# Optimization experiments

Hardware: AMD Instinct MI355X
Metric: run time of the kernel (lower is better)

Reference implementation:

```python
import jax, jax.numpy as jnp
import numpy as np
from jax import lax

C = 256
HEADS = 8
HD = C // HEADS  # 32
D = 32  # max(L=32, C//16)
KERNELS = [1, 3, 5, 7]
EPS = 1e-5


def setup_inputs() -> dict:
    key = jax.random.key(0)
    ks = jax.random.split(key, 16)
    inp = {
        'x': jax.random.normal(ks[0], (8, C, 32, 32), jnp.float32),
        'qkv_w': jax.random.normal(ks[1], (3 * C, C), jnp.float32) * 0.05,
        'out_w': jax.random.normal(ks[2], (C, C), jnp.float32) * 0.05,
        'conv_w1': jax.random.normal(ks[3], (C, C, 1, 1), jnp.float32) * 0.05,
        'conv_w3': jax.random.normal(ks[4], (C, C, 3, 3), jnp.float32) * 0.05,
        'conv_w5': jax.random.normal(ks[5], (C, C, 5, 5), jnp.float32) * 0.05,
        'conv_w7': jax.random.normal(ks[6], (C, C, 7, 7), jnp.float32) * 0.05,
        'conv_b': jax.random.normal(ks[7], (4, C), jnp.float32) * 0.05,
        'bn_gamma': jax.random.uniform(ks[8], (4, C), jnp.float32, 0.5, 1.5),
        'bn_beta': jax.random.normal(ks[9], (4, C), jnp.float32) * 0.05,
        'bn_mean': jax.random.normal(ks[10], (4, C), jnp.float32) * 0.05,
        'bn_var': jax.random.uniform(ks[11], (4, C), jnp.float32, 0.5, 1.5),
        'fc_w': jax.random.normal(ks[12], (D, C), jnp.float32) * 0.05,
        'fc_b': jax.random.normal(ks[13], (D,), jnp.float32) * 0.05,
        'fcs_w': jax.random.normal(ks[14], (4, C, D), jnp.float32) * 0.05,
        'fcs_b': jax.random.normal(ks[15], (4, C), jnp.float32) * 0.05,
    }
    return inp


def _conv_bn_relu(x, w, b, g, beta, m, v):
    k = w.shape[-1]
    y = lax.conv_general_dilated(
        x, w, window_strides=(1, 1), padding=[(k // 2, k // 2)] * 2,
        dimension_numbers=('NCHW', 'OIHW', 'NCHW'))
    y = y + b[None, :, None, None]
    inv = g / jnp.sqrt(v + EPS)  # eval-mode batchnorm
    y = y * inv[None, :, None, None] + (beta - m * inv)[None, :, None, None]
    return jax.nn.relu(y)


def reference(x, qkv_w, out_w, conv_w1, conv_w3, conv_w5, conv_w7, conv_b,
              bn_gamma, bn_beta, bn_mean, bn_var, fc_w, fc_b, fcs_w, fcs_b):
    bsz, ch, ht, wd = x.shape
    n = ht * wd
    xf = x.reshape(bsz, ch, n)
    qkv = jnp.einsum('oc,bcn->bon', qkv_w, xf)  # [b, 3C, N] (1x1 conv)
    q, k, v = jnp.split(qkv, 3, axis=1)
    q = q.reshape(bsz, HEADS, HD, n)
    k = k.reshape(bsz, HEADS, HD, n)
    v = v.reshape(bsz, HEADS, HD, n)
    scale = 1.0 / np.sqrt(HD)
    scores = jnp.einsum('bhdi,bhdj->bhij', q, k) * scale  # [b,h,N,N]
    probs = jax.nn.softmax(scores, axis=-1)
    ctx = jnp.einsum('bhij,bhdj->bhdi', probs, v)  # [b,h,hd,N]
    ctx = ctx.reshape(bsz, ch, ht, wd)
    out = jnp.einsum('oc,bcn->bon', out_w, ctx.reshape(bsz, ch, n)).reshape(bsz, ch, ht, wd)

    ws = [conv_w1, conv_w3, conv_w5, conv_w7]
    feats = jnp.stack([
        _conv_bn_relu(out, ws[i], conv_b[i], bn_gamma[i], bn_beta[i], bn_mean[i], bn_var[i])
        for i in range(4)
    ], axis=0)  # [4, b, C, H, W]
    U = feats.sum(axis=0)
    S = U.mean(axis=(-2, -1))  # [b, C]
    Z = S @ fc_w.T + fc_b  # [b, D]
    logits = jnp.einsum('kcd,bd->kbc', fcs_w, Z) + fcs_b[:, None, :]  # [4,b,C]
    attn = jax.nn.softmax(logits, axis=0)[:, :, :, None, None]  # softmax over kernel branches
    V = (attn * feats).sum(axis=0)  # [b, C, H, W]
    return V
```

## Files before the change

kernel.cpp:

```cpp
#include <hip/hip_runtime.h>
#include <math.h>


typedef __attribute__((ext_vector_type(8))) short bf16x8;
typedef __attribute__((ext_vector_type(4))) float f32x4;

__device__ __forceinline__ ushort f2bf(float f) {
  uint32_t u = __float_as_uint(f);
  u += 0x7fffu + ((u >> 16) & 1u);
  return (ushort)(u >> 16);
}

__device__ __forceinline__ uint cvt_pk(float lo, float hi) {
  uint r;
  asm volatile("v_cvt_pk_bf16_f32 %0, %1, %2" : "=v"(r) : "v"(lo), "v"(hi));
  return r;
}


template <int KK>
__device__ __forceinline__ void repack_dev(const float* __restrict__ src,
                                           ushort* __restrict__ dst, int M, int co,
                                           char* smraw) {
  ushort(*t)[KK + 1] = (ushort(*)[KK + 1])smraw;
  int tid = threadIdx.x;
  for (int idx = tid; idx < 256 * KK; idx += 256) {
    int ci = idx / KK, k = idx - ci * KK;
    t[ci][k] = f2bf(src[(size_t)co * 256 * KK + idx]);
  }
  __syncthreads();
  for (int idx = tid; idx < 256 * KK; idx += 256) {
    int k = idx >> 8, ci = idx & 255;
    dst[((size_t)k * M + co) * 256 + ci] = t[ci][k];
  }
}

__device__ __forceinline__ void pad_dev(const float* __restrict__ src,
                                        ushort* __restrict__ dst, int y, int b,
                                        char* smraw) {
  ushort(*t)[258] = (ushort(*)[258])smraw;
  int tid = threadIdx.x;
  for (int u = 0; u < 32; ++u) {
    int idx = u * 256 + tid;
    int c = idx >> 5, p = idx & 31;
    t[p][c] = f2bf(src[(((size_t)b * 256 + c) << 10) + (y << 5) + p]);
  }
  __syncthreads();
  for (int u = 0; u < 32; ++u) {
    int idx = u * 256 + tid;
    int p = idx >> 8, c = idx & 255;
    dst[(((size_t)b * 38 + y + 3) * 38 + p + 3) * 256 + c] = t[p][c];
  }
}

__global__ __launch_bounds__(256) void prep_all(
    const float* __restrict__ qkv_w, const float* __restrict__ out_w,
    const float* __restrict__ cw1, const float* __restrict__ cw3,
    const float* __restrict__ cw5, const float* __restrict__ cw7,
    ushort* __restrict__ Wq, ushort* __restrict__ Wo, ushort* __restrict__ Wc,
    const float* __restrict__ x, ushort* __restrict__ P1,
    const float* __restrict__ cb, const float* __restrict__ g,
    const float* __restrict__ be, const float* __restrict__ mn,
    const float* __restrict__ v, float* __restrict__ binv, float* __restrict__ bb2) {
  __shared__ __align__(16) char sm[25600];
  int gx = blockIdx.x;
  if (gx < 768) repack_dev<1>(qkv_w, Wq, 768, gx, sm);
  else if (gx < 1024) repack_dev<1>(out_w, Wo, 256, gx - 768, sm);
  else if (gx < 1280) repack_dev<1>(cw1, Wc, 256, gx - 1024, sm);
  else if (gx < 1536) repack_dev<9>(cw3, Wc + 65536, 256, gx - 1280, sm);
  else if (gx < 1792) repack_dev<25>(cw5, Wc + 655360, 256, gx - 1536, sm);
  else if (gx < 2048) repack_dev<49>(cw7, Wc + 2293760, 256, gx - 1792, sm);
  else if (gx < 2304) pad_dev(x, P1, (gx - 2048) & 31, (gx - 2048) >> 5, sm);
  else {
    int tid = threadIdx.x;
#pragma unroll
    for (int u = 0; u < 4; ++u) {
      int i = u * 256 + tid;
      float inv = g[i] * rsqrtf(v[i] + 1e-5f);
      binv[i] = inv;
      bb2[i] = be[i] + (cb[i] - mn[i]) * inv;
    }
  }
}

template <int MODE>
__device__ __forceinline__ void conv_core(
    const ushort* __restrict__ W, const ushort* __restrict__ X,
    float* __restrict__ outF, ushort* __restrict__ outU,
    int M, int KS, int b, int co0, int pxt, int cs0, int cs1, bool accum,
    char* smem) {
  const int R = KS >> 1;
  const int NT = KS * KS;
  const int NR = 4 + 2 * R;
  const int NPIX = NR * 38;
  char* Bs = smem;
  char* As = smem + 24320;
  const int tid = threadIdx.x;
  const int w = tid >> 6, l = tid & 63, lr = l & 15, sg = l >> 4;
  const int y0 = pxt * 4;
  const ushort* Xb = X + ((size_t)b * 38 + (y0 + 3 - R)) * 38 * 256;

  f32x4 acc[4][4] = {};

  auto stageA = [&](int t, int ci0, int bufsel) {
    const ushort* Wt = W + ((size_t)t * M + co0) * 256 + ci0;
    char* dbase = As + (bufsel << 13) + (w << 11);
#pragma unroll
    for (int u = 0; u < 2; ++u) {
      int idx16 = (w * 2 + u) * 64 + l;
      int co = idx16 >> 2, s = idx16 & 3;
      const ushort* src = Wt + (size_t)co * 256 + ((s ^ ((co >> 1) & 3)) << 3);
      __builtin_amdgcn_global_load_lds(
          (const __attribute__((address_space(1))) void*)src,
          (__attribute__((address_space(3))) void*)(dbase + (u << 10)), 16, 0, 0);
    }
  };

  int g = 0;
  stageA(0, cs0 << 5, 0);
  const int u_stg = (NPIX * 4 + 255) >> 8;
  for (int cs = cs0; cs < cs1; ++cs) {
    int ci0 = cs << 5;
    for (int u = 0; u < u_stg; ++u) {
      int idx = (u << 8) + tid;
      if (idx < NPIX * 4) {
        int pix = idx >> 2, s = idx & 3;
        int pr = pix / 38, pc = pix - pr * 38;
        const ushort* srcp = Xb + ((size_t)(pr * 38 + pc)) * 256 + ci0 +
                             ((s ^ ((pc >> 1) & 3)) << 3);
        __builtin_amdgcn_global_load_lds(
            (const __attribute__((address_space(1))) void*)srcp,
            (__attribute__((address_space(3))) void*)(Bs + (u << 12) + (w << 10)),
            16, 0, 0);
      }
    }
    __syncthreads();
    int dy = 0, dx = 0;
    for (int t = 0; t < NT; ++t) {
      bool staged = true;
      if (t + 1 < NT) stageA(t + 1, ci0, (g + 1) & 1);
      else if (cs + 1 < cs1) stageA(0, ci0 + 32, (g + 1) & 1);
      else staged = false;
      if (staged)
        asm volatile("s_waitcnt vmcnt(2)\n\ts_barrier" ::: "memory");
      else
        asm volatile("s_waitcnt vmcnt(0)\n\ts_barrier" ::: "memory");

      bf16x8 af[4], bfr[4];
      char* Ab = As + ((g & 1) << 13);
#pragma unroll
      for (int fa = 0; fa < 4; ++fa) {
        int co = (w & 1) * 64 + fa * 16 + lr;
        af[fa] = *(const bf16x8*)(Ab + (co << 6) + ((sg ^ ((co >> 1) & 3)) << 4));
      }
      int rowbase = (w >> 1) * 2 + dy;
      int cbase = dx + 3 - R + lr;
#pragma unroll
      for (int fp = 0; fp < 4; ++fp) {
        int lrow = rowbase + (fp >> 1);
        int pc = cbase + ((fp & 1) << 4);
        bfr[fp] = *(const bf16x8*)(Bs + ((lrow * 38 + pc) << 6) +
                                   ((sg ^ ((pc >> 1) & 3)) << 4));
      }
      __builtin_amdgcn_s_setprio(1);
#pragma unroll
      for (int fa = 0; fa < 4; ++fa)
#pragma unroll
        for (int fp = 0; fp < 4; ++fp)
          acc[fa][fp] = __builtin_amdgcn_mfma_f32_16x16x32_bf16(
              af[fa], bfr[fp], acc[fa][fp], 0, 0, 0);
      __builtin_amdgcn_s_setprio(0);
      ++g;
      if (++dx == KS) { dx = 0; ++dy; }
      asm volatile("s_barrier" ::: "memory");
    }
  }
  int coB = co0 + (w & 1) * 64;
  int pxB = pxt * 128 + (w >> 1) * 64;
#pragma unroll
  for (int fa = 0; fa < 4; ++fa) {
#pragma unroll
    for (int fp = 0; fp < 4; ++fp) {
      int px = pxB + (fp >> 1) * 32 + (fp & 1) * 16 + lr;
      int cobase = coB + fa * 16 + 4 * sg;
      f32x4 v4 = acc[fa][fp];
      if (MODE == 2) {
#pragma unroll
        for (int r = 0; r < 4; ++r) {
          int co = cobase + r;
          float* dst = &outF[((size_t)b * M + co) * 1024 + px];
          if (accum) unsafeAtomicAdd(dst, v4[r]);
          else *dst = v4[r];
        }
      } else if (MODE == 1) {
        int y = px >> 5, x = px & 31;
        ushort* dst = outU + ((size_t)(b * 38 + y + 3) * 38 + x + 3) * 256 + cobase;
        *(uint*)dst = cvt_pk(v4[0], v4[1]);
        *(uint*)(dst + 2) = cvt_pk(v4[2], v4[3]);
      } else {
        if (coB < 256) {
          int h = cobase >> 5, d = cobase & 31;
          ushort* dst = outU + ((size_t)(b * 8 + h) * 1024 + px) * 32 + d;
          const float sc = 0.17677669529663687f;
          *(uint*)dst = cvt_pk(v4[0] * sc, v4[1] * sc);
          *(uint*)(dst + 2) = cvt_pk(v4[2] * sc, v4[3] * sc);
        } else if (coB < 512) {
          int c2 = cobase - 256;
          int h = c2 >> 5, d = c2 & 31;
          ushort* dst = outU + 2097152 + ((size_t)(b * 8 + h) * 1024 + px) * 32 + d;
          *(uint*)dst = cvt_pk(v4[0], v4[1]);
          *(uint*)(dst + 2) = cvt_pk(v4[2], v4[3]);
        } else {
          int c2 = cobase - 512;
#pragma unroll
          for (int r = 0; r < 4; ++r)
            outU[4194304 + ((size_t)(b * 256 + c2 + r)) * 1024 + px] = f2bf(v4[r]);
        }
      }
    }
  }
}

__global__ __launch_bounds__(256, 2) void gemm_qkv(const ushort* __restrict__ W,
                                                   const ushort* __restrict__ X,
                                                   ushort* __restrict__ U) {
  __shared__ __align__(16) char smem[40704];
  int cot = blockIdx.x >> 3, pxt = blockIdx.x & 7, b = blockIdx.y;
  conv_core<0>(W, X, nullptr, U, 768, 1, b, cot * 128, pxt, 0, 8, false, smem);
}

__global__ __launch_bounds__(256, 2) void gemm_oproj(const ushort* __restrict__ W,
                                                     const ushort* __restrict__ X,
                                                     ushort* __restrict__ U) {
  __shared__ __align__(16) char smem[40704];
  int cot = blockIdx.x >> 3, pxt = blockIdx.x & 7, b = blockIdx.y;
  conv_core<1>(W, X, nullptr, U, 256, 1, b, cot * 128, pxt, 0, 8, false, smem);
}

__global__ __launch_bounds__(256, 4) void conv_fused(const ushort* __restrict__ Wc,
                                                     const ushort* __restrict__ X,
                                                     float* __restrict__ feats) {
  __shared__ __align__(16) char smem[40704];
  int gx = blockIdx.x;
  int sub = gx & 127;
  int pxt = sub & 7, cot = (sub >> 3) & 1, b = sub >> 4;
  int br, cs0, cs1;
  if (gx < 512) {
    br = 3; int ch = gx >> 7; cs0 = ch * 2; cs1 = cs0 + 2;
  } else if (gx < 768) {
    br = 2; int ch = (gx >> 7) & 1; cs0 = ch * 4; cs1 = cs0 + 4;
  } else {
    br = 1; int ch = (gx >> 7) & 1; cs0 = ch * 4; cs1 = cs0 + 4;
  }
  const int ksarr[4] = {1, 3, 5, 7};
  const int wofs[4] = {0, 65536, 655360, 2293760};
  conv_core<2>(Wc + wofs[br], X, feats + (size_t)br * 2097152, nullptr, 256,
               ksarr[br], b, cot * 128, pxt, cs0, cs1, true, smem);
  if (gx >= 768 && gx < 896) {
    __syncthreads();
    conv_core<2>(Wc, X, feats, nullptr, 256, 1, b, cot * 128, pxt, 0, 8, false,
                 smem);
  }
}

__global__ __launch_bounds__(256, 2) void flash_attn(const ushort* __restrict__ QKV,
                                                     ushort* __restrict__ P2out) {
  __shared__ __align__(16) char smem[24576];
  const int tid = threadIdx.x, w = tid >> 6, l = tid & 63, lr = l & 15, sg = l >> 4;
  char* Ks = smem;
  char* Vs = smem + 4096;
  char* Ps = smem + 8192 + (w << 12);
  int bh = blockIdx.y, b = bh >> 3, h = bh & 7;
  const ushort* QT = QKV + (size_t)bh * 32768;
  const ushort* KT = QKV + 2097152 + (size_t)bh * 32768;
  const ushort* VT = QKV + 4194304 + (size_t)(b * 256 + h * 32) * 1024;
  int ibase = blockIdx.x * 128 + w * 32;

  bf16x8 qf[2];
#pragma unroll
  for (int i16 = 0; i16 < 2; ++i16)
    qf[i16] = *(const bf16x8*)(QT + ((size_t)(ibase + i16 * 16 + lr)) * 32 + sg * 8);

  f32x4 oacc[4] = {};
  float mrow[2] = {-3e30f, -3e30f};
  float lrow[2] = {0.f, 0.f};

  for (int jb = 0; jb < 1024; jb += 64) {
    {
      int j = tid >> 2, s = tid & 3;
      const ushort* srcK = KT + (size_t)(jb + j) * 32 + ((s ^ ((j >> 1) & 3)) << 3);
      __builtin_amdgcn_global_load_lds(
          (const __attribute__((address_space(1))) void*)srcK,
          (__attribute__((address_space(3))) void*)(Ks + (w << 10)), 16, 0, 0);
      int d = tid >> 3, s2 = tid & 7;
      const ushort* srcV = VT + (size_t)d * 1024 + jb + ((s2 ^ (d & 7)) << 3);
      __builtin_amdgcn_global_load_lds(
          (const __attribute__((address_space(1))) void*)srcV,
          (__attribute__((address_space(3))) void*)(Vs + (w << 10)), 16, 0, 0);
    }
    __syncthreads();

    bf16x8 kf[4];
#pragma unroll
    for (int jt = 0; jt < 4; ++jt) {
      int j = jt * 16 + lr;
      kf[jt] = *(const bf16x8*)(Ks + j * 64 + ((sg ^ ((j >> 1) & 3)) << 4));
    }
    f32x4 sac[2][4] = {};
#pragma unroll
    for (int i16 = 0; i16 < 2; ++i16)
#pragma unroll
      for (int jt = 0; jt < 4; ++jt)
        sac[i16][jt] = __builtin_amdgcn_mfma_f32_16x16x32_bf16(
            kf[jt], qf[i16], sac[i16][jt], 0, 0, 0);

#pragma unroll
    for (int i16 = 0; i16 < 2; ++i16) {
      float tmax = sac[i16][0][0];
#pragma unroll
      for (int jt = 0; jt < 4; ++jt)
#pragma unroll
        for (int r = 0; r < 4; ++r) tmax = fmaxf(tmax, sac[i16][jt][r]);
      tmax = fmaxf(tmax, __shfl_xor(tmax, 16));
      tmax = fmaxf(tmax, __shfl_xor(tmax, 32));
      float mnew = fmaxf(mrow[i16], tmax);
      float fac = __expf(mrow[i16] - mnew);
      mrow[i16] = mnew;
      float psum = 0.f;
      int i = i16 * 16 + lr;
      char* prow = Ps + i * 128;
#pragma unroll
      for (int jt = 0; jt < 4; ++jt) {
        float p0 = __expf(sac[i16][jt][0] - mnew);
        float p1 = __expf(sac[i16][jt][1] - mnew);
        float p2 = __expf(sac[i16][jt][2] - mnew);
        float p3 = __expf(sac[i16][jt][3] - mnew);
        psum += (p0 + p1) + (p2 + p3);
        int j0 = jt * 16 + sg * 4;
        uint* dst = (uint*)(prow + (((j0 >> 3) ^ (i & 7)) << 4) + ((j0 & 7) << 1));
        dst[0] = cvt_pk(p0, p1);
        dst[1] = cvt_pk(p2, p3);
      }
      lrow[i16] = lrow[i16] * fac + psum;
#pragma unroll
      for (int d16 = 0; d16 < 2; ++d16)
#pragma unroll
        for (int r = 0; r < 4; ++r) oacc[d16 * 2 + i16][r] *= fac;
    }
    asm volatile("s_waitcnt lgkmcnt(0)" ::: "memory");

#pragma unroll
    for (int h2 = 0; h2 < 2; ++h2) {
      bf16x8 vf[2], pf[2];
#pragma unroll
      for (int d16 = 0; d16 < 2; ++d16) {
        int d = d16 * 16 + lr;
        vf[d16] = *(const bf16x8*)(Vs + d * 128 + ((((h2 << 2) + sg) ^ (d & 7)) << 4));
      }
#pragma unroll
      for (int i16 = 0; i16 < 2; ++i16) {
        int i = i16 * 16 + lr;
        pf[i16] = *(const bf16x8*)(Ps + i * 128 + ((((h2 << 2) + sg) ^ (i & 7)) << 4));
      }
#pragma unroll
      for (int d16 = 0; d16 < 2; ++d16)
#pragma unroll
        for (int i16 = 0; i16 < 2; ++i16)
          oacc[d16 * 2 + i16] = __builtin_amdgcn_mfma_f32_16x16x32_bf16(
              vf[d16], pf[i16], oacc[d16 * 2 + i16], 0, 0, 0);
    }
    __syncthreads();
  }

  float linv[2];
#pragma unroll
  for (int i16 = 0; i16 < 2; ++i16) {
    float lt = lrow[i16];
    lt += __shfl_xor(lt, 16);
    lt += __shfl_xor(lt, 32);
    linv[i16] = 1.0f / lt;
  }
#pragma unroll
  for (int i16 = 0; i16 < 2; ++i16) {
    int i = ibase + i16 * 16 + lr;
    int y = i >> 5, x = i & 31;
    ushort* dst0 = P2out + ((size_t)(b * 38 + y + 3) * 38 + x + 3) * 256 + h * 32 + sg * 4;
#pragma unroll
    for (int d16 = 0; d16 < 2; ++d16) {
      f32x4 v = oacc[d16 * 2 + i16];
      ushort* dst = dst0 + d16 * 16;
      *(uint*)dst = cvt_pk(v[0] * linv[i16], v[1] * linv[i16]);
      *(uint*)(dst + 2) = cvt_pk(v[2] * linv[i16], v[3] * linv[i16]);
    }
  }
}

__global__ __launch_bounds__(256) void reduce_s(const float* __restrict__ feats,
                                                const float* __restrict__ binv,
                                                const float* __restrict__ bb2,
                                                float* __restrict__ S) {
  int bc = blockIdx.x;
  int c = bc & 255;
  const float* p = feats + (size_t)bc * 1024;
  float s = 0;
#pragma unroll
  for (int k = 0; k < 4; ++k) {
    float bi = binv[k * 256 + c], bo = bb2[k * 256 + c];
#pragma unroll
    for (int u = 0; u < 4; ++u)
      s += fmaxf(fmaf(p[(size_t)k * 2097152 + u * 256 + threadIdx.x], bi, bo), 0.f);
  }
  __shared__ float red[256];
  red[threadIdx.x] = s;
  __syncthreads();
  for (int off = 128; off > 0; off >>= 1) {
    if (threadIdx.x < off) red[threadIdx.x] += red[threadIdx.x + off];
    __syncthreads();
  }
  if (threadIdx.x == 0) S[bc] = red[0] * (1.0f / 1024.0f);
}

__global__ __launch_bounds__(256) void fc_attn_k(
    const float* __restrict__ S, const float* __restrict__ fc_w,
    const float* __restrict__ fc_b, const float* __restrict__ fcs_w,
    const float* __restrict__ fcs_b, float* __restrict__ attnw) {
  int b = blockIdx.x;
  __shared__ float Ss[256];
  __shared__ float Zs[32];
  int tid = threadIdx.x;
  Ss[tid] = S[b * 256 + tid];
  __syncthreads();
  if (tid < 32) {
    float z = fc_b[tid];
    for (int c = 0; c < 256; ++c) z += Ss[c] * fc_w[tid * 256 + c];
    Zs[tid] = z;
  }
  __syncthreads();
  int c = tid;
  float lg[4];
#pragma unroll
  for (int k = 0; k < 4; ++k) {
    float v = fcs_b[k * 256 + c];
    const float* wp = &fcs_w[((size_t)k * 256 + c) * 32];
#pragma unroll
    for (int d = 0; d < 32; ++d) v += wp[d] * Zs[d];
    lg[k] = v;
  }
  float m = fmaxf(fmaxf(lg[0], lg[1]), fmaxf(lg[2], lg[3]));
  float e0 = __expf(lg[0] - m), e1 = __expf(lg[1] - m);
  float e2 = __expf(lg[2] - m), e3 = __expf(lg[3] - m);
  float inv = 1.0f / (e0 + e1 + e2 + e3);
  attnw[(0 * 8 + b) * 256 + c] = e0 * inv;
  attnw[(1 * 8 + b) * 256 + c] = e1 * inv;
  attnw[(2 * 8 + b) * 256 + c] = e2 * inv;
  attnw[(3 * 8 + b) * 256 + c] = e3 * inv;
}

__global__ __launch_bounds__(256) void combine_k(const float* __restrict__ feats,
                                                 const float* __restrict__ attnw,
                                                 const float* __restrict__ binv,
                                                 const float* __restrict__ bb2,
                                                 float* __restrict__ out) {
  size_t idx = (size_t)blockIdx.x * 256 + threadIdx.x;
  int c = (int)((idx >> 10) & 255);
  int b = (int)(idx >> 18);
  float s = 0;
#pragma unroll
  for (int k = 0; k < 4; ++k) {
    float v = fmaxf(fmaf(feats[(size_t)k * 2097152 + idx],
                         binv[k * 256 + c], bb2[k * 256 + c]), 0.f);
    s += attnw[(k * 8 + b) * 256 + c] * v;
  }
  out[idx] = s;
}

extern "C" void kernel_launch(void* const* d_in, const int* in_sizes, int n_in,
                              void* d_out, int out_size, void* d_ws, size_t ws_size,
                              hipStream_t stream) {
  (void)in_sizes; (void)n_in; (void)out_size; (void)ws_size;
  const float* x      = (const float*)d_in[0];
  const float* qkv_w  = (const float*)d_in[1];
  const float* out_w  = (const float*)d_in[2];
  const float* cw1    = (const float*)d_in[3];
  const float* cw3    = (const float*)d_in[4];
  const float* cw5    = (const float*)d_in[5];
  const float* cw7    = (const float*)d_in[6];
  const float* conv_b = (const float*)d_in[7];
  const float* bn_g   = (const float*)d_in[8];
  const float* bn_b   = (const float*)d_in[9];
  const float* bn_m   = (const float*)d_in[10];
  const float* bn_v   = (const float*)d_in[11];
  const float* fc_w   = (const float*)d_in[12];
  const float* fc_b   = (const float*)d_in[13];
  const float* fcs_w  = (const float*)d_in[14];
  const float* fcs_b  = (const float*)d_in[15];

  char*  wsb   = (char*)d_ws;
  float* wsf   = (float*)d_ws;
  ushort* QKVb = (ushort*)d_ws;
  float* feats = wsf;
  float* S     = wsf + 10485760;
  float* attnw = wsf + 10487808;
  ushort* P1   = (ushort*)(wsb + 41984000);
  ushort* P2   = (ushort*)(wsb + 47898624);
  ushort* Wq   = (ushort*)(wsb + 53813248);
  ushort* Wo   = (ushort*)(wsb + 54206464);
  ushort* Wc   = (ushort*)(wsb + 54337536);
  float* binv  = (float*)(wsb + 65347584);
  float* bb2   = (float*)(wsb + 65351680);
  float* out   = (float*)d_out;

  hipMemsetAsync(P1, 0, 2 * 5914624, stream);
  hipMemsetAsync(wsb + 16777216, 0, 16777216, stream);
  prep_all<<<2305, 256, 0, stream>>>(qkv_w, out_w, cw1, cw3, cw5, cw7, Wq, Wo, Wc,
                                     x, P1, conv_b, bn_g, bn_b, bn_m, bn_v, binv,
                                     bb2);

  gemm_qkv<<<dim3(48, 8), 256, 0, stream>>>(Wq, P1, QKVb);
  flash_attn<<<dim3(8, 64), 256, 0, stream>>>(QKVb, P2);
  hipMemsetAsync(wsb + 8388608, 0, 8388608, stream);
  gemm_oproj<<<dim3(16, 8), 256, 0, stream>>>(Wo, P2, P1);
  conv_fused<<<dim3(1024), 256, 0, stream>>>(Wc, P1, feats);

  reduce_s<<<2048, 256, 0, stream>>>(feats, binv, bb2, S);
  fc_attn_k<<<8, 256, 0, stream>>>(S, fc_w, fc_b, fcs_w, fcs_b, attnw);
  combine_k<<<8192, 256, 0, stream>>>(feats, attnw, binv, bb2, out);
}
```

Measured before the change: 221.3 us.

## Fuse all conv branches per channel slice, reuse staged input tile, vectorize epilogues

conv_fused now splits work by 32-channel input slice. Each block stages the 7x7-halo input tile once and runs all four kernel-size branches over it, prefetching the next branch's weights. Partial results are atomically added into each branch's feature plane. This replaces the old uneven branch and channel split, which restaged inputs per branch. The two large memsets of padded buffers are replaced by a border-only zeroing pass inside prep_all plus a single workspace memset. reduce_s and combine_k move to float4 loads. The trade-off is more atomic traffic, since all four branches are now split eight ways, and a longer serial loop per block.

New measurement: 336.5 us. +52.1%, slower.

```diff
diff --git a/kernel.cpp b/kernel.cpp
--- a/kernel.cpp
+++ b/kernel.cpp
@@ -58,7 +58,7 @@
     const float* __restrict__ cw1, const float* __restrict__ cw3,
     const float* __restrict__ cw5, const float* __restrict__ cw7,
     ushort* __restrict__ Wq, ushort* __restrict__ Wo, ushort* __restrict__ Wc,
-    const float* __restrict__ x, ushort* __restrict__ P1,
+    const float* __restrict__ x, ushort* __restrict__ P1, ushort* __restrict__ P2,
     const float* __restrict__ cb, const float* __restrict__ g,
     const float* __restrict__ be, const float* __restrict__ mn,
     const float* __restrict__ v, float* __restrict__ binv, float* __restrict__ bb2) {
@@ -71,7 +71,7 @@
   else if (gx < 1792) repack_dev<25>(cw5, Wc + 655360, 256, gx - 1536, sm);
   else if (gx < 2048) repack_dev<49>(cw7, Wc + 2293760, 256, gx - 1792, sm);
   else if (gx < 2304) pad_dev(x, P1, (gx - 2048) & 31, (gx - 2048) >> 5, sm);
-  else {
+  else if (gx == 2304) {
     int tid = threadIdx.x;
 #pragma unroll
     for (int u = 0; u < 4; ++u) {
@@ -80,15 +80,37 @@
       binv[i] = inv;
       bb2[i] = be[i] + (cb[i] - mn[i]) * inv;
     }
+  } else {
+    int z = gx - 2305;
+    int bufb = z >> 3;
+    int part = z & 7;
+    ushort* base = (bufb < 8 ? P1 : P2) + (size_t)(bufb & 7) * 369664;
+    uint4* b4 = (uint4*)base;
+    uint4 z4; z4.x = z4.y = z4.z = z4.w = 0u;
+    for (int q = 0; q < 7; ++q) {
+      int idx = q * 256 + threadIdx.x;
+      if (idx < 1680) {
+        int uidx = part * 1680 + idx;
+        int p = uidx >> 5, ch = uidx & 31;
+        int y, xx;
+        if (p < 114) { y = p / 38; xx = p - y * 38; }
+        else if (p < 306) {
+          int r = p - 114; int ry = r / 6; int xi = r - ry * 6;
+          y = 3 + ry; xx = xi < 3 ? xi : xi + 32;
+        } else {
+          int r = p - 306; int ry = r / 38; y = 35 + ry; xx = r - ry * 38;
+        }
+        b4[(y * 38 + xx) * 32 + ch] = z4;
+      }
+    }
   }
 }
 
 template <int MODE>
 __device__ __forceinline__ void conv_core(
     const ushort* __restrict__ W, const ushort* __restrict__ X,
-    float* __restrict__ outF, ushort* __restrict__ outU,
-    int M, int KS, int b, int co0, int pxt, int cs0, int cs1, bool accum,
-    char* smem) {
+    ushort* __restrict__ outU, int M, int KS, int b, int co0, int pxt,
+    int cs0, int cs1, char* smem) {
   const int R = KS >> 1;
   const int NT = KS * KS;
   const int NR = 4 + 2 * R;
@@ -184,15 +206,7 @@
       int px = pxB + (fp >> 1) * 32 + (fp & 1) * 16 + lr;
       int cobase = coB + fa * 16 + 4 * sg;
       f32x4 v4 = acc[fa][fp];
-      if (MODE == 2) {
-#pragma unroll
-        for (int r = 0; r < 4; ++r) {
-          int co = cobase + r;
-          float* dst = &outF[((size_t)b * M + co) * 1024 + px];
-          if (accum) unsafeAtomicAdd(dst, v4[r]);
-          else *dst = v4[r];
-        }
-      } else if (MODE == 1) {
+      if (MODE == 1) {
         int y = px >> 5, x = px & 31;
         ushort* dst = outU + ((size_t)(b * 38 + y + 3) * 38 + x + 3) * 256 + cobase;
         *(uint*)dst = cvt_pk(v4[0], v4[1]);
@@ -226,7 +240,7 @@
                                                    ushort* __restrict__ U) {
   __shared__ __align__(16) char smem[40704];
   int cot = blockIdx.x >> 3, pxt = blockIdx.x & 7, b = blockIdx.y;
-  conv_core<0>(W, X, nullptr, U, 768, 1, b, cot * 128, pxt, 0, 8, false, smem);
+  conv_core<0>(W, X, U, 768, 1, b, cot * 128, pxt, 0, 8, smem);
 }
 
 __global__ __launch_bounds__(256, 2) void gemm_oproj(const ushort* __restrict__ W,
@@ -234,32 +248,123 @@
                                                      ushort* __restrict__ U) {
   __shared__ __align__(16) char smem[40704];
   int cot = blockIdx.x >> 3, pxt = blockIdx.x & 7, b = blockIdx.y;
-  conv_core<1>(W, X, nullptr, U, 256, 1, b, cot * 128, pxt, 0, 8, false, smem);
+  conv_core<1>(W, X, U, 256, 1, b, cot * 128, pxt, 0, 8, smem);
 }
 
 __global__ __launch_bounds__(256, 4) void conv_fused(const ushort* __restrict__ Wc,
                                                      const ushort* __restrict__ X,
                                                      float* __restrict__ feats) {
   __shared__ __align__(16) char smem[40704];
-  int gx = blockIdx.x;
-  int sub = gx & 127;
-  int pxt = sub & 7, cot = (sub >> 3) & 1, b = sub >> 4;
-  int br, cs0, cs1;
-  if (gx < 512) {
-    br = 3; int ch = gx >> 7; cs0 = ch * 2; cs1 = cs0 + 2;
-  } else if (gx < 768) {
-    br = 2; int ch = (gx >> 7) & 1; cs0 = ch * 4; cs1 = cs0 + 4;
-  } else {
-    br = 1; int ch = (gx >> 7) & 1; cs0 = ch * 4; cs1 = cs0 + 4;
-  }
-  const int ksarr[4] = {1, 3, 5, 7};
-  const int wofs[4] = {0, 65536, 655360, 2293760};
-  conv_core<2>(Wc + wofs[br], X, feats + (size_t)br * 2097152, nullptr, 256,
-               ksarr[br], b, cot * 128, pxt, cs0, cs1, true, smem);
-  if (gx >= 768 && gx < 896) {
-    __syncthreads();
-    conv_core<2>(Wc, X, feats, nullptr, 256, 1, b, cot * 128, pxt, 0, 8, false,
-                 smem);
+  char* Bs = smem;
+  char* As = smem + 24320;
+  const int gx = blockIdx.x;
+  const int cs = gx >> 7, sub = gx & 127;
+  const int pxt = sub & 7, cot = (sub >> 3) & 1, b = sub >> 4;
+  const int co0 = cot * 128, ci0 = cs << 5;
+  const int tid = threadIdx.x;
+  const int w = tid >> 6, l = tid & 63, lr = l & 15, sg = l >> 4;
+  const int y0 = pxt * 4;
+  const ushort* Xb = X + ((size_t)b * 38 + y0) * 38 * 256;
+
+  auto stageA = [&](const ushort* Wb, int t, int bufsel) {
+    const ushort* Wt = Wb + ((size_t)t * 256 + co0) * 256 + ci0;
+    char* dbase = As + (bufsel << 13) + (w << 11);
+#pragma unroll
+    for (int u = 0; u < 2; ++u) {
+      int idx16 = (w * 2 + u) * 64 + l;
+      int co = idx16 >> 2, s = idx16 & 3;
+      const ushort* src = Wt + (size_t)co * 256 + ((s ^ ((co >> 1) & 3)) << 3);
+      __builtin_amdgcn_global_load_lds(
+          (const __attribute__((address_space(1))) void*)src,
+          (__attribute__((address_space(3))) void*)(dbase + (u << 10)), 16, 0, 0);
+    }
+  };
+
+  f32x4 acc[4][4] = {};
+  stageA(Wc + 2293760, 0, 0);
+#pragma unroll
+  for (int u = 0; u < 6; ++u) {
+    int idx = (u << 8) + tid;
+    if (idx < 1520) {
+      int pix = idx >> 2, s = idx & 3;
+      int pr = pix / 38, pc = pix - pr * 38;
+      const ushort* srcp = Xb + ((size_t)(pr * 38 + pc)) * 256 + ci0 +
+                           ((s ^ ((pc >> 1) & 3)) << 3);
+      __builtin_amdgcn_global_load_lds(
+          (const __attribute__((address_space(1))) void*)srcp,
+          (__attribute__((address_space(3))) void*)(Bs + (u << 12) + (w << 10)),
+          16, 0, 0);
+    }
+  }
+  __syncthreads();
+
+  int g = 0;
+#pragma unroll
+  for (int bi = 0; bi < 4; ++bi) {
+    const int KS = (bi == 0) ? 7 : (bi == 1) ? 5 : (bi == 2) ? 3 : 1;
+    const int R = KS >> 1;
+    const int NT = KS * KS;
+    const ushort* Wb =
+        Wc + ((bi == 0) ? 2293760 : (bi == 1) ? 655360 : (bi == 2) ? 65536 : 0);
+    const ushort* Wnext =
+        Wc + ((bi == 0) ? 655360 : (bi == 1) ? 65536 : 0);
+    int dy = 0, dx = 0;
+#pragma unroll 1
+    for (int t = 0; t < NT; ++t) {
+      bool staged = true;
+      if (t + 1 < NT) stageA(Wb, t + 1, (g + 1) & 1);
+      else if (bi + 1 < 4) stageA(Wnext, 0, (g + 1) & 1);
+      else staged = false;
+      if (staged)
+        asm volatile("s_waitcnt vmcnt(2)\n\ts_barrier" ::: "memory");
+      else
+        asm volatile("s_waitcnt vmcnt(0)\n\ts_barrier" ::: "memory");
+
+      bf16x8 af[4], bfr[4];
+      char* Ab = As + ((g & 1) << 13);
+#pragma unroll
+      for (int fa = 0; fa < 4; ++fa) {
+        int co = (w & 1) * 64 + fa * 16 + lr;
+        af[fa] = *(const bf16x8*)(Ab + (co << 6) + ((sg ^ ((co >> 1) & 3)) << 4));
+      }
+      int rowbase = (w >> 1) * 2 + dy + (3 - R);
+      int cbase = dx + 3 - R + lr;
+#pragma unroll
+      for (int fp = 0; fp < 4; ++fp) {
+        int lrow = rowbase + (fp >> 1);
+        int pc = cbase + ((fp & 1) << 4);
+        bfr[fp] = *(const bf16x8*)(Bs + ((lrow * 38 + pc) << 6) +
+                                   ((sg ^ ((pc >> 1) & 3)) << 4));
+      }
+      __builtin_amdgcn_s_setprio(1);
+#pragma unroll
+      for (int fa = 0; fa < 4; ++fa)
+#pragma unroll
+        for (int fp = 0; fp < 4; ++fp)
+          acc[fa][fp] = __builtin_amdgcn_mfma_f32_16x16x32_bf16(
+              af[fa], bfr[fp], acc[fa][fp], 0, 0, 0);
+      __builtin_amdgcn_s_setprio(0);
+      ++g;
+      if (++dx == KS) { dx = 0; ++dy; }
+      asm volatile("s_barrier" ::: "memory");
+    }
+    float* plane = feats + (size_t)(3 - bi) * 2097152;
+    int coB = co0 + (w & 1) * 64;
+    int pxB = pxt * 128 + (w >> 1) * 64;
+#pragma unroll
+    for (int fa = 0; fa < 4; ++fa) {
+#pragma unroll
+      for (int fp = 0; fp < 4; ++fp) {
+        int px = pxB + (fp >> 1) * 32 + (fp & 1) * 16 + lr;
+        int cobase = coB + fa * 16 + 4 * sg;
+        f32x4 v4 = acc[fa][fp];
+#pragma unroll
+        for (int r = 0; r < 4; ++r)
+          unsafeAtomicAdd(&plane[((size_t)b * 256 + cobase + r) * 1024 + px], v4[r]);
+#pragma unroll
+        for (int r = 0; r < 4; ++r) acc[fa][fp][r] = 0.f;
+      }
+    }
   }
 }
 
@@ -401,14 +506,14 @@
                                                 float* __restrict__ S) {
   int bc = blockIdx.x;
   int c = bc & 255;
-  const float* p = feats + (size_t)bc * 1024;
+  const float4* p4 = (const float4*)feats + (size_t)bc * 256;
   float s = 0;
 #pragma unroll
   for (int k = 0; k < 4; ++k) {
     float bi = binv[k * 256 + c], bo = bb2[k * 256 + c];
-#pragma unroll
-    for (int u = 0; u < 4; ++u)
-      s += fmaxf(fmaf(p[(size_t)k * 2097152 + u * 256 + threadIdx.x], bi, bo), 0.f);
+    float4 v = p4[(size_t)k * 524288 + threadIdx.x];
+    s += fmaxf(fmaf(v.x, bi, bo), 0.f) + fmaxf(fmaf(v.y, bi, bo), 0.f) +
+         fmaxf(fmaf(v.z, bi, bo), 0.f) + fmaxf(fmaf(v.w, bi, bo), 0.f);
   }
   __shared__ float red[256];
   red[threadIdx.x] = s;
@@ -461,17 +566,21 @@
                                                  const float* __restrict__ binv,
                                                  const float* __restrict__ bb2,
                                                  float* __restrict__ out) {
-  size_t idx = (size_t)blockIdx.x * 256 + threadIdx.x;
-  int c = (int)((idx >> 10) & 255);
-  int b = (int)(idx >> 18);
-  float s = 0;
+  size_t i4 = (size_t)blockIdx.x * 256 + threadIdx.x;
+  int c = (int)((i4 >> 8) & 255);
+  int b = (int)(i4 >> 16);
+  float4 s = {0.f, 0.f, 0.f, 0.f};
 #pragma unroll
   for (int k = 0; k < 4; ++k) {
-    float v = fmaxf(fmaf(feats[(size_t)k * 2097152 + idx],
-                         binv[k * 256 + c], bb2[k * 256 + c]), 0.f);
-    s += attnw[(k * 8 + b) * 256 + c] * v;
-  }
-  out[idx] = s;
+    float bi = binv[k * 256 + c], bo = bb2[k * 256 + c];
+    float aw = attnw[(k * 8 + b) * 256 + c];
+    float4 v = ((const float4*)feats)[(size_t)k * 524288 + i4];
+    s.x += aw * fmaxf(fmaf(v.x, bi, bo), 0.f);
+    s.y += aw * fmaxf(fmaf(v.y, bi, bo), 0.f);
+    s.z += aw * fmaxf(fmaf(v.z, bi, bo), 0.f);
+    s.w += aw * fmaxf(fmaf(v.w, bi, bo), 0.f);
+  }
+  ((float4*)out)[i4] = s;
 }
 
 extern "C" void kernel_launch(void* const* d_in, const int* in_sizes, int n_in,
@@ -510,19 +619,17 @@
   float* bb2   = (float*)(wsb + 65351680);
   float* out   = (float*)d_out;
 
-  hipMemsetAsync(P1, 0, 2 * 5914624, stream);
-  hipMemsetAsync(wsb + 16777216, 0, 16777216, stream);
-  prep_all<<<2305, 256, 0, stream>>>(qkv_w, out_w, cw1, cw3, cw5, cw7, Wq, Wo, Wc,
-                                     x, P1, conv_b, bn_g, bn_b, bn_m, bn_v, binv,
-                                     bb2);
+  prep_all<<<2433, 256, 0, stream>>>(qkv_w, out_w, cw1, cw3, cw5, cw7, Wq, Wo, Wc,
+                                     x, P1, P2, conv_b, bn_g, bn_b, bn_m, bn_v,
+                                     binv, bb2);
 
   gemm_qkv<<<dim3(48, 8), 256, 0, stream>>>(Wq, P1, QKVb);
   flash_attn<<<dim3(8, 64), 256, 0, stream>>>(QKVb, P2);
-  hipMemsetAsync(wsb + 8388608, 0, 8388608, stream);
+  hipMemsetAsync(d_ws, 0, 33554432, stream);
   gemm_oproj<<<dim3(16, 8), 256, 0, stream>>>(Wo, P2, P1);
   conv_fused<<<dim3(1024), 256, 0, stream>>>(Wc, P1, feats);
 
   reduce_s<<<2048, 256, 0, stream>>>(feats, binv, bb2, S);
   fc_attn_k<<<8, 256, 0, stream>>>(S, fc_w, fc_b, fcs_w, fcs_b, attnw);
-  combine_k<<<8192, 256, 0, stream>>>(feats, attnw, binv, bb2, out);
-}
+  combine_k<<<2048, 256, 0, stream>>>(feats, attnw, binv, bb2, out);
+}
```
